# Kernel tuning notes

Measured on AMD Instinct MI355X. Metric: run time of the kernel, lower is better.

The kernel has to match this reference:

```python
import jax, jax.numpy as jnp
import numpy as np

N_NODES = 100000


def _prep(edge_index, n, dtype):
    # Add self-loops and compute GCN symmetric normalization (edge_weight = 1).
    loop = jnp.arange(n)
    src = jnp.concatenate([edge_index[0], loop])
    dst = jnp.concatenate([edge_index[1], loop])
    ones = jnp.ones(src.shape[0], dtype)
    deg = jax.ops.segment_sum(ones, dst, num_segments=n)  # in-degree over col, incl. self-loop
    dinv = jnp.where(deg > 0, 1.0 / jnp.sqrt(deg), 0.0)
    norm = dinv[src] * dinv[dst]  # per-edge deg^-1/2 * deg^-1/2
    cnt = jnp.maximum(deg, 1.0)   # incoming-edge count for aggr='mean' (weights are 1)
    return src, dst, norm, cnt


def _gcn_conv(h, W, b, src, dst, norm, cnt, n):
    # gather -> scale -> scatter-mean  (PyG GCNConv with aggr='mean')
    msg = norm[:, None] * (h @ W)[src]                      # [E+N, out]
    agg = jax.ops.segment_sum(msg, dst, num_segments=n)     # [N, out]
    return agg / cnt[:, None] + b


def setup_inputs() -> dict:
    key = jax.random.key(0)
    ks = jax.random.split(key, 8)
    n, d_in, d_h, d_out = N_NODES, 128, 128, 64
    x = jax.random.normal(ks[0], (n, d_in), dtype=jnp.float32)
    edge_index = jax.random.randint(ks[1], (2, 1600000), 0, n, dtype=jnp.int64)
    def glorot(k, fan_in, fan_out):
        s = jnp.sqrt(6.0 / (fan_in + fan_out)).astype(jnp.float32)
        return jax.random.uniform(k, (fan_in, fan_out), jnp.float32, -s, s)
    return {
        "x": x,
        "edge_index": edge_index,
        "W1": glorot(ks[2], d_in, d_h), "b1": jnp.zeros((d_h,), jnp.float32),
        "W2": glorot(ks[3], d_h, d_h), "b2": jnp.zeros((d_h,), jnp.float32),
        "W3": glorot(ks[4], d_h, d_out), "b3": jnp.zeros((d_out,), jnp.float32),
    }


def reference(x, edge_index, W1, b1, W2, b2, W3, b3):
    n = x.shape[0]
    src, dst, norm, cnt = _prep(edge_index, n, x.dtype)
    h = jax.nn.relu(_gcn_conv(x, W1, b1, src, dst, norm, cnt, n))  # dropout = identity (eval)
    h = jax.nn.relu(_gcn_conv(h, W2, b2, src, dst, norm, cnt, n))
    out = _gcn_conv(h, W3, b3, src, dst, norm, cnt, n)
    return out
```

## Files before the change

### kernel.cpp

```cpp
#include <hip/hip_runtime.h>
#include <hip/hip_fp16.h>
#include <math.h>


#define BLK 256

__global__ void init_and_pad(int* __restrict__ deg, int n,
                             int* __restrict__ colidx, int val, int len) {
    int i = blockIdx.x * blockDim.x + threadIdx.x;
    int stride = gridDim.x * blockDim.x;
    for (; i < len; i += stride) {
        if (i < n) deg[i] = 1;
        colidx[i] = val;
    }
}

__global__ void count_deg_rank(const int* __restrict__ dst, int* __restrict__ deg,
                               int* __restrict__ rank, int E) {
    int e = blockIdx.x * blockDim.x + threadIdx.x;
    if (e < E) {
        int old = atomicAdd(&deg[dst[e]], 1);
        rank[e] = old - 1;
    }
}

__device__ __forceinline__ int padcap(int d) { return (d - 1 + 7) & ~7; }

__global__ void scan_block_sums(const int* __restrict__ deg, int* __restrict__ bsum, int n) {
    __shared__ int s[BLK];
    int i = blockIdx.x * BLK + threadIdx.x;
    s[threadIdx.x] = (i < n) ? padcap(deg[i]) : 0;
    __syncthreads();
    for (int off = BLK / 2; off > 0; off >>= 1) {
        if (threadIdx.x < off) s[threadIdx.x] += s[threadIdx.x + off];
        __syncthreads();
    }
    if (threadIdx.x == 0) bsum[blockIdx.x] = s[0];
}

__global__ void scan_partials_excl(int* __restrict__ bsum, int nb) {
    __shared__ int a[512];
    __shared__ int b[512];
    int t = threadIdx.x;
    int v = (t < nb) ? bsum[t] : 0;
    a[t] = v;
    __syncthreads();
    int* s = a; int* d = b;
    for (int off = 1; off < 512; off <<= 1) {
        int val = s[t];
        if (t >= off) val += s[t - off];
        d[t] = val;
        __syncthreads();
        int* tmp = s; s = d; d = tmp;
    }
    if (t < nb) bsum[t] = s[t] - v;
}

__global__ void scan_write_rowptr(const int* __restrict__ deg, const int* __restrict__ bsum,
                                  int* __restrict__ rowptr, float* __restrict__ dinv, int n) {
    __shared__ int a[BLK];
    __shared__ int b[BLK];
    int t = threadIdx.x;
    int i = blockIdx.x * BLK + t;
    int dgv = (i < n) ? deg[i] : 1;
    int v = (i < n) ? padcap(dgv) : 0;
    a[t] = v;
    __syncthreads();
    int* s = a; int* d = b;
    for (int off = 1; off < BLK; off <<= 1) {
        int val = s[t];
        if (t >= off) val += s[t - off];
        d[t] = val;
        __syncthreads();
        int* tmp = s; s = d; d = tmp;
    }
    if (i < n) {
        rowptr[i] = (s[t] - v) + bsum[blockIdx.x];
        dinv[i] = 1.0f / sqrtf((float)dgv);
    }
}

__global__ void place_edges(const int* __restrict__ src, const int* __restrict__ dst,
                            const int* __restrict__ rowptr, const int* __restrict__ rank,
                            int* __restrict__ colidx, int E) {
    int e = blockIdx.x * blockDim.x + threadIdx.x;
    if (e < E) {
        int d = dst[e];
        colidx[rowptr[d] + rank[e]] = src[e];
    }
}

template <int KOUT>
__global__ __launch_bounds__(256) void gemm_tiled(const float* __restrict__ H,
                                                  const float* __restrict__ W,
                                                  const float* __restrict__ dinv,
                                                  __half* __restrict__ Y, int n) {
    constexpr int ROWS = (KOUT == 128) ? 64 : 128;
    constexpr int HSTR = 36;
    __shared__ float Hl[ROWS][HSTR];
    __shared__ float Wl[32][KOUT];

    const int t = threadIdx.x;
    const int wave = t >> 6, lane = t & 63;
    const int rg = lane >> 3;
    const int cg = lane & 7;
    const int rpanel = (KOUT == 128) ? (wave >> 1) : wave;
    const int cpanel = (KOUT == 128) ? (wave & 1) : 0;
    const int row0 = blockIdx.x * ROWS;
    const int cbase = cpanel * 64 + cg * 8;

    if (blockIdx.x == 0 && t < KOUT) Y[(size_t)n * KOUT + t] = __float2half(0.f);

    float acc[4][8];
#pragma unroll
    for (int i = 0; i < 4; i++)
#pragma unroll
        for (int j = 0; j < 8; j++) acc[i][j] = 0.f;

    for (int kt = 0; kt < 128; kt += 32) {
#pragma unroll
        for (int s = 0; s < ROWS / 32; s++) {
            int r = s * 32 + (t >> 3);
            int kk = (t & 7) * 4;
            int row = row0 + r;
            float4 v = make_float4(0.f, 0.f, 0.f, 0.f);
            if (row < n) v = *(const float4*)(H + (size_t)row * 128 + kt + kk);
            Hl[r][kk] = v.x; Hl[r][kk + 1] = v.y; Hl[r][kk + 2] = v.z; Hl[r][kk + 3] = v.w;
        }
        {
            const float* Wg = W + (size_t)kt * KOUT;
            float* Wf = &Wl[0][0];
            for (int idx = t * 4; idx < 32 * KOUT; idx += 1024) {
                *(float4*)(Wf + idx) = *(const float4*)(Wg + idx);
            }
        }
        __syncthreads();

#pragma unroll 2
        for (int kk = 0; kk < 32; kk += 4) {
            float4 a[4];
#pragma unroll
            for (int i = 0; i < 4; i++)
                a[i] = *(const float4*)(&Hl[rpanel * 32 + rg + 8 * i][kk]);
#pragma unroll
            for (int q = 0; q < 4; q++) {
                float4 w0 = *(const float4*)(&Wl[kk + q][cbase]);
                float4 w1 = *(const float4*)(&Wl[kk + q][cbase + 4]);
#pragma unroll
                for (int i = 0; i < 4; i++) {
                    float av = (q == 0) ? a[i].x : (q == 1) ? a[i].y : (q == 2) ? a[i].z : a[i].w;
                    acc[i][0] += av * w0.x; acc[i][1] += av * w0.y;
                    acc[i][2] += av * w0.z; acc[i][3] += av * w0.w;
                    acc[i][4] += av * w1.x; acc[i][5] += av * w1.y;
                    acc[i][6] += av * w1.z; acc[i][7] += av * w1.w;
                }
            }
        }
        __syncthreads();
    }

#pragma unroll
    for (int i = 0; i < 4; i++) {
        int row = row0 + rpanel * 32 + rg + 8 * i;
        if (row < n) {
            float dv = dinv[row];
            __half hv[8];
#pragma unroll
            for (int j = 0; j < 8; j++) hv[j] = __float2half_rn(dv * acc[i][j]);
            *(uint4*)(Y + (size_t)row * KOUT + cbase) = *(const uint4*)hv;
        }
    }
}

__device__ __forceinline__ int sel4(const int4 v, int q) {
    return (q == 0) ? v.x : (q == 1) ? v.y : (q == 2) ? v.z : v.w;
}

__device__ __forceinline__ void acc_half8(float* __restrict__ acc, const __half* __restrict__ p) {
    uint4 u = *(const uint4*)p;
    const __half2* h = (const __half2*)&u;
    float2 f0 = __half22float2(h[0]);
    float2 f1 = __half22float2(h[1]);
    float2 f2 = __half22float2(h[2]);
    float2 f3 = __half22float2(h[3]);
    acc[0] += f0.x; acc[1] += f0.y; acc[2] += f1.x; acc[3] += f1.y;
    acc[4] += f2.x; acc[5] += f2.y; acc[6] += f3.x; acc[7] += f3.y;
}

template <bool RELU>
__global__ __launch_bounds__(256) void agg128(const __half* __restrict__ Ys,
                                              const int* __restrict__ rowptr,
                                              const int* __restrict__ deg,
                                              const float* __restrict__ dinv,
                                              const int* __restrict__ colidx,
                                              const float* __restrict__ bias,
                                              float* __restrict__ out, int n) {
    int wid = (blockIdx.x * blockDim.x + threadIdx.x) >> 6;
    int lane = threadIdx.x & 63;
    if (wid >= n) return;
    const int q = lane >> 4;
    const int l4 = lane & 15;

    int start = __builtin_amdgcn_readfirstlane(rowptr[wid]);
    int dg    = __builtin_amdgcn_readfirstlane(deg[wid]);
    int mpad  = padcap(dg);
    float di = dinv[wid];

    float acc[8];
#pragma unroll
    for (int j = 0; j < 8; j++) acc[j] = 0.f;
    if (q == 0) acc_half8(acc, Ys + ((size_t)wid << 7) + l4 * 8);

    const int4* cp4 = (const int4*)(colidx + start);
    for (int j = 0; j < mpad; j += 8) {
        int4 a = cp4[j >> 2];
        int4 b = cp4[(j >> 2) + 1];
        int s0 = sel4(a, q);
        int s1 = sel4(b, q);
        acc_half8(acc, Ys + ((size_t)s0 << 7) + l4 * 8);
        acc_half8(acc, Ys + ((size_t)s1 << 7) + l4 * 8);
    }
#pragma unroll
    for (int j = 0; j < 8; j++) {
        acc[j] += __shfl_xor(acc[j], 16);
        acc[j] += __shfl_xor(acc[j], 32);
    }

    if (q == 0) {
        float scale = di / (float)dg;
        float4 b0 = *(const float4*)(bias + l4 * 8);
        float4 b1 = *(const float4*)(bias + l4 * 8 + 4);
        float o[8];
        o[0] = acc[0] * scale + b0.x; o[1] = acc[1] * scale + b0.y;
        o[2] = acc[2] * scale + b0.z; o[3] = acc[3] * scale + b0.w;
        o[4] = acc[4] * scale + b1.x; o[5] = acc[5] * scale + b1.y;
        o[6] = acc[6] * scale + b1.z; o[7] = acc[7] * scale + b1.w;
        if (RELU) {
#pragma unroll
            for (int j = 0; j < 8; j++) o[j] = fmaxf(o[j], 0.f);
        }
        float* op = out + ((size_t)wid << 7) + l4 * 8;
        *(float4*)op = make_float4(o[0], o[1], o[2], o[3]);
        *(float4*)(op + 4) = make_float4(o[4], o[5], o[6], o[7]);
    }
}

template <bool RELU>
__global__ __launch_bounds__(256) void agg64(const __half* __restrict__ Ys,
                                             const int* __restrict__ rowptr,
                                             const int* __restrict__ deg,
                                             const float* __restrict__ dinv,
                                             const int* __restrict__ colidx,
                                             const float* __restrict__ bias,
                                             float* __restrict__ out, int n) {
    int wid = (blockIdx.x * blockDim.x + threadIdx.x) >> 6;
    int lane = threadIdx.x & 63;
    if (wid >= n) return;
    const int oct = lane >> 3;
    const int l3 = lane & 7;

    int start = __builtin_amdgcn_readfirstlane(rowptr[wid]);
    int dg    = __builtin_amdgcn_readfirstlane(deg[wid]);
    int mpad  = padcap(dg);
    float di = dinv[wid];

    float acc[8];
#pragma unroll
    for (int j = 0; j < 8; j++) acc[j] = 0.f;
    if (oct == 0) acc_half8(acc, Ys + ((size_t)wid << 6) + l3 * 8);

    const int4* cp4 = (const int4*)(colidx + start);
    for (int j = 0; j < mpad; j += 8) {
        int4 a = cp4[j >> 2];
        int4 b = cp4[(j >> 2) + 1];
        int se = (oct < 4) ? sel4(a, oct) : sel4(b, oct - 4);
        acc_half8(acc, Ys + ((size_t)se << 6) + l3 * 8);
    }
#pragma unroll
    for (int j = 0; j < 8; j++) {
        acc[j] += __shfl_xor(acc[j], 8);
        acc[j] += __shfl_xor(acc[j], 16);
        acc[j] += __shfl_xor(acc[j], 32);
    }

    if (oct == 0) {
        float scale = di / (float)dg;
        float4 b0 = *(const float4*)(bias + l3 * 8);
        float4 b1 = *(const float4*)(bias + l3 * 8 + 4);
        float o[8];
        o[0] = acc[0] * scale + b0.x; o[1] = acc[1] * scale + b0.y;
        o[2] = acc[2] * scale + b0.z; o[3] = acc[3] * scale + b0.w;
        o[4] = acc[4] * scale + b1.x; o[5] = acc[5] * scale + b1.y;
        o[6] = acc[6] * scale + b1.z; o[7] = acc[7] * scale + b1.w;
        if (RELU) {
#pragma unroll
            for (int j = 0; j < 8; j++) o[j] = fmaxf(o[j], 0.f);
        }
        float* op = out + ((size_t)wid << 6) + l3 * 8;
        *(float4*)op = make_float4(o[0], o[1], o[2], o[3]);
        *(float4*)(op + 4) = make_float4(o[4], o[5], o[6], o[7]);
    }
}

extern "C" void kernel_launch(void* const* d_in, const int* in_sizes, int n_in,
                              void* d_out, int out_size, void* d_ws, size_t ws_size,
                              hipStream_t stream) {
    const float* x  = (const float*)d_in[0];
    const int*   ei = (const int*)d_in[1];
    const float* W1 = (const float*)d_in[2];
    const float* b1 = (const float*)d_in[3];
    const float* W2 = (const float*)d_in[4];
    const float* b2 = (const float*)d_in[5];
    const float* W3 = (const float*)d_in[6];
    const float* b3 = (const float*)d_in[7];
    float* out = (float*)d_out;

    const int n = in_sizes[0] / 128;
    const int E = in_sizes[1] / 2;
    const int* srcA = ei;
    const int* dstA = ei + E;
    const int Epad = E + 8 * n + 64;

    auto alignup = [](size_t v) { return (v + 255) & ~(size_t)255; };
    char* base = (char*)d_ws;
    size_t off = 0;
    int* deg    = (int*)(base + off); off = alignup(off + (size_t)n * 4);
    int* rank   = (int*)(base + off); off = alignup(off + (size_t)E * 4);
    int* rowptr = (int*)(base + off); off = alignup(off + (size_t)n * 4);
    int* bsum   = (int*)(base + off); off = alignup(off + (size_t)1024 * 4);
    int* colidx = (int*)(base + off); off = alignup(off + (size_t)Epad * 4);
    float* dinv = (float*)(base + off); off = alignup(off + (size_t)n * 4);
    float* Hb   = (float*)(base + off); off = alignup(off + (size_t)n * 128 * 4);
    __half* Yb  = (__half*)(base + off); off = alignup(off + (size_t)(n + 1) * 128 * 2);
    (void)ws_size;

    const int nbN = (n + BLK - 1) / BLK;
    const int nbE = (E + BLK - 1) / BLK;

    init_and_pad<<<2048, BLK, 0, stream>>>(deg, n, colidx, n, Epad);
    count_deg_rank<<<nbE, BLK, 0, stream>>>(dstA, deg, rank, E);
    scan_block_sums<<<nbN, BLK, 0, stream>>>(deg, bsum, n);
    scan_partials_excl<<<1, 512, 0, stream>>>(bsum, nbN);
    scan_write_rowptr<<<nbN, BLK, 0, stream>>>(deg, bsum, rowptr, dinv, n);
    place_edges<<<nbE, BLK, 0, stream>>>(srcA, dstA, rowptr, rank, colidx, E);

    const int aggBlocks = (n * 64 + BLK - 1) / BLK;

    gemm_tiled<128><<<(n + 63) / 64, 256, 0, stream>>>(x, W1, dinv, Yb, n);
    agg128<true><<<aggBlocks, BLK, 0, stream>>>(Yb, rowptr, deg, dinv, colidx, b1, Hb, n);

    gemm_tiled<128><<<(n + 63) / 64, 256, 0, stream>>>(Hb, W2, dinv, Yb, n);
    agg128<true><<<aggBlocks, BLK, 0, stream>>>(Yb, rowptr, deg, dinv, colidx, b2, Hb, n);

    gemm_tiled<64><<<(n + 127) / 128, 256, 0, stream>>>(Hb, W3, dinv, Yb, n);
    agg64<false><<<aggBlocks, BLK, 0, stream>>>(Yb, rowptr, deg, dinv, colidx, b3, out, n);
}
```

Measured before the change: 409.0 us.

## Use bf16 MFMA GEMMs, bf16 hidden activations, and batch atomic edge kernels

Replaces the FP32 tiled GEMMs with bf16 MFMA 16x16x32 kernels that read weights pre-transposed and cast by a new setup kernel. Hidden activations between layers are now stored as bf16 instead of fp32, which halves their memory traffic. The degree-count and edge-placement kernels now handle four edges per thread so more atomics and scattered loads are in flight at once. Rounding inputs and weights to bf16 lowers GEMM accuracy, and the MFMA epilogue writes scalar half values instead of vector stores.

```diff
diff --git a/kernel.cpp b/kernel.cpp
--- a/kernel.cpp
+++ b/kernel.cpp
@@ -4,6 +4,15 @@
 
 
 #define BLK 256
+
+typedef short bf16x8 __attribute__((ext_vector_type(8)));
+typedef float f32x4 __attribute__((ext_vector_type(4)));
+
+__device__ __forceinline__ unsigned short f2bf(float f) {
+    unsigned int u = __float_as_uint(f);
+    u += 0x7fffu + ((u >> 16) & 1u);
+    return (unsigned short)(u >> 16);
+}
 
 __global__ void init_and_pad(int* __restrict__ deg, int n,
                              int* __restrict__ colidx, int val, int len) {
@@ -15,13 +24,41 @@
     }
 }
 
+__global__ void transpose_cast_w3(const float* __restrict__ W1, const float* __restrict__ W2,
+                                  const float* __restrict__ W3, unsigned short* __restrict__ Wt1,
+                                  unsigned short* __restrict__ Wt2, unsigned short* __restrict__ Wt3) {
+    int idx = blockIdx.x * blockDim.x + threadIdx.x;
+    if (idx < 16384) {
+        int k = idx >> 7, c = idx & 127;
+        Wt1[c * 128 + k] = f2bf(W1[idx]);
+    } else if (idx < 32768) {
+        int j = idx - 16384; int k = j >> 7, c = j & 127;
+        Wt2[c * 128 + k] = f2bf(W2[j]);
+    } else if (idx < 40960) {
+        int j = idx - 32768; int k = j >> 6, c = j & 63;
+        Wt3[c * 128 + k] = f2bf(W3[j]);
+    }
+}
+
 __global__ void count_deg_rank(const int* __restrict__ dst, int* __restrict__ deg,
                                int* __restrict__ rank, int E) {
-    int e = blockIdx.x * blockDim.x + threadIdx.x;
-    if (e < E) {
-        int old = atomicAdd(&deg[dst[e]], 1);
-        rank[e] = old - 1;
-    }
+    int t = blockIdx.x * blockDim.x + threadIdx.x;
+    int s = gridDim.x * blockDim.x;
+    int e0 = t, e1 = t + s, e2 = t + 2 * s, e3 = t + 3 * s;
+    int d0 = 0, d1 = 0, d2 = 0, d3 = 0;
+    if (e0 < E) d0 = dst[e0];
+    if (e1 < E) d1 = dst[e1];
+    if (e2 < E) d2 = dst[e2];
+    if (e3 < E) d3 = dst[e3];
+    int r0 = 0, r1 = 0, r2 = 0, r3 = 0;
+    if (e0 < E) r0 = atomicAdd(&deg[d0], 1);
+    if (e1 < E) r1 = atomicAdd(&deg[d1], 1);
+    if (e2 < E) r2 = atomicAdd(&deg[d2], 1);
+    if (e3 < E) r3 = atomicAdd(&deg[d3], 1);
+    if (e0 < E) rank[e0] = r0 - 1;
+    if (e1 < E) rank[e1] = r1 - 1;
+    if (e2 < E) rank[e2] = r2 - 1;
+    if (e3 < E) rank[e3] = r3 - 1;
 }
 
 __device__ __forceinline__ int padcap(int d) { return (d - 1 + 7) & ~7; }
@@ -83,91 +120,95 @@
 __global__ void place_edges(const int* __restrict__ src, const int* __restrict__ dst,
                             const int* __restrict__ rowptr, const int* __restrict__ rank,
                             int* __restrict__ colidx, int E) {
-    int e = blockIdx.x * blockDim.x + threadIdx.x;
-    if (e < E) {
-        int d = dst[e];
-        colidx[rowptr[d] + rank[e]] = src[e];
-    }
-}
-
-template <int KOUT>
-__global__ __launch_bounds__(256) void gemm_tiled(const float* __restrict__ H,
-                                                  const float* __restrict__ W,
-                                                  const float* __restrict__ dinv,
-                                                  __half* __restrict__ Y, int n) {
-    constexpr int ROWS = (KOUT == 128) ? 64 : 128;
-    constexpr int HSTR = 36;
-    __shared__ float Hl[ROWS][HSTR];
-    __shared__ float Wl[32][KOUT];
-
+    int t = blockIdx.x * blockDim.x + threadIdx.x;
+    int s = gridDim.x * blockDim.x;
+    int e0 = t, e1 = t + s, e2 = t + 2 * s, e3 = t + 3 * s;
+    int d0 = 0, d1 = 0, d2 = 0, d3 = 0;
+    if (e0 < E) d0 = dst[e0];
+    if (e1 < E) d1 = dst[e1];
+    if (e2 < E) d2 = dst[e2];
+    if (e3 < E) d3 = dst[e3];
+    int p0 = 0, p1 = 0, p2 = 0, p3 = 0;
+    if (e0 < E) p0 = rowptr[d0] + rank[e0];
+    if (e1 < E) p1 = rowptr[d1] + rank[e1];
+    if (e2 < E) p2 = rowptr[d2] + rank[e2];
+    if (e3 < E) p3 = rowptr[d3] + rank[e3];
+    if (e0 < E) colidx[p0] = src[e0];
+    if (e1 < E) colidx[p1] = src[e1];
+    if (e2 < E) colidx[p2] = src[e2];
+    if (e3 < E) colidx[p3] = src[e3];
+}
+
+template <int KOUT, bool INF32>
+__global__ __launch_bounds__(256) void gemm_mfma(const void* __restrict__ Hv,
+                                                 const unsigned short* __restrict__ Wt,
+                                                 const float* __restrict__ dinv,
+                                                 __half* __restrict__ Y, int n) {
+    constexpr int NCH = KOUT / 16;
+    __shared__ unsigned short Hl[64][136];
+    __shared__ unsigned short Wl[KOUT][136];
     const int t = threadIdx.x;
+    const int row0 = blockIdx.x * 64;
+
+    for (int idx = t; idx < KOUT * 16; idx += 256) {
+        int r = idx >> 4, seg = idx & 15;
+        *(uint4*)&Wl[r][seg * 8] = *(const uint4*)(Wt + r * 128 + seg * 8);
+    }
+    if (INF32) {
+        const float* H = (const float*)Hv;
+        for (int idx = t; idx < 64 * 16; idx += 256) {
+            int r = idx >> 4, seg = idx & 15;
+            int row = row0 + r;
+            unsigned short tmp[8];
+            if (row < n) {
+                float4 v0 = *(const float4*)(H + (size_t)row * 128 + seg * 8);
+                float4 v1 = *(const float4*)(H + (size_t)row * 128 + seg * 8 + 4);
+                tmp[0] = f2bf(v0.x); tmp[1] = f2bf(v0.y); tmp[2] = f2bf(v0.z); tmp[3] = f2bf(v0.w);
+                tmp[4] = f2bf(v1.x); tmp[5] = f2bf(v1.y); tmp[6] = f2bf(v1.z); tmp[7] = f2bf(v1.w);
+            } else {
+#pragma unroll
+                for (int j = 0; j < 8; j++) tmp[j] = 0;
+            }
+            *(uint4*)&Hl[r][seg * 8] = *(const uint4*)tmp;
+        }
+    } else {
+        const unsigned short* H = (const unsigned short*)Hv;
+        for (int idx = t; idx < 64 * 16; idx += 256) {
+            int r = idx >> 4, seg = idx & 15;
+            int row = row0 + r;
+            uint4 v = make_uint4(0, 0, 0, 0);
+            if (row < n) v = *(const uint4*)(H + (size_t)row * 128 + seg * 8);
+            *(uint4*)&Hl[r][seg * 8] = v;
+        }
+    }
+    if (blockIdx.x == 0 && t < KOUT) Y[(size_t)n * KOUT + t] = __float2half(0.f);
+    __syncthreads();
+
     const int wave = t >> 6, lane = t & 63;
-    const int rg = lane >> 3;
-    const int cg = lane & 7;
-    const int rpanel = (KOUT == 128) ? (wave >> 1) : wave;
-    const int cpanel = (KOUT == 128) ? (wave & 1) : 0;
-    const int row0 = blockIdx.x * ROWS;
-    const int cbase = cpanel * 64 + cg * 8;
-
-    if (blockIdx.x == 0 && t < KOUT) Y[(size_t)n * KOUT + t] = __float2half(0.f);
-
-    float acc[4][8];
-#pragma unroll
-    for (int i = 0; i < 4; i++)
-#pragma unroll
-        for (int j = 0; j < 8; j++) acc[i][j] = 0.f;
-
-    for (int kt = 0; kt < 128; kt += 32) {
-#pragma unroll
-        for (int s = 0; s < ROWS / 32; s++) {
-            int r = s * 32 + (t >> 3);
-            int kk = (t & 7) * 4;
-            int row = row0 + r;
-            float4 v = make_float4(0.f, 0.f, 0.f, 0.f);
-            if (row < n) v = *(const float4*)(H + (size_t)row * 128 + kt + kk);
-            Hl[r][kk] = v.x; Hl[r][kk + 1] = v.y; Hl[r][kk + 2] = v.z; Hl[r][kk + 3] = v.w;
+    const int r16 = lane & 15, ko8 = (lane >> 4) * 8;
+    f32x4 acc[NCH];
+#pragma unroll
+    for (int c = 0; c < NCH; c++) acc[c] = (f32x4){0.f, 0.f, 0.f, 0.f};
+
+#pragma unroll
+    for (int kc = 0; kc < 4; kc++) {
+        bf16x8 a = *(const bf16x8*)&Hl[wave * 16 + r16][kc * 32 + ko8];
+#pragma unroll
+        for (int c = 0; c < NCH; c++) {
+            bf16x8 b = *(const bf16x8*)&Wl[c * 16 + r16][kc * 32 + ko8];
+            acc[c] = __builtin_amdgcn_mfma_f32_16x16x32_bf16(a, b, acc[c], 0, 0, 0);
         }
-        {
-            const float* Wg = W + (size_t)kt * KOUT;
-            float* Wf = &Wl[0][0];
-            for (int idx = t * 4; idx < 32 * KOUT; idx += 1024) {
-                *(float4*)(Wf + idx) = *(const float4*)(Wg + idx);
-            }
-        }
-        __syncthreads();
-
-#pragma unroll 2
-        for (int kk = 0; kk < 32; kk += 4) {
-            float4 a[4];
-#pragma unroll
-            for (int i = 0; i < 4; i++)
-                a[i] = *(const float4*)(&Hl[rpanel * 32 + rg + 8 * i][kk]);
-#pragma unroll
-            for (int q = 0; q < 4; q++) {
-                float4 w0 = *(const float4*)(&Wl[kk + q][cbase]);
-                float4 w1 = *(const float4*)(&Wl[kk + q][cbase + 4]);
-#pragma unroll
-                for (int i = 0; i < 4; i++) {
-                    float av = (q == 0) ? a[i].x : (q == 1) ? a[i].y : (q == 2) ? a[i].z : a[i].w;
-                    acc[i][0] += av * w0.x; acc[i][1] += av * w0.y;
-                    acc[i][2] += av * w0.z; acc[i][3] += av * w0.w;
-                    acc[i][4] += av * w1.x; acc[i][5] += av * w1.y;
-                    acc[i][6] += av * w1.z; acc[i][7] += av * w1.w;
-                }
-            }
-        }
-        __syncthreads();
-    }
-
-#pragma unroll
-    for (int i = 0; i < 4; i++) {
-        int row = row0 + rpanel * 32 + rg + 8 * i;
+    }
+
+    const int mbase = row0 + wave * 16 + (lane >> 4) * 4;
+#pragma unroll
+    for (int r = 0; r < 4; r++) {
+        int row = mbase + r;
         if (row < n) {
             float dv = dinv[row];
-            __half hv[8];
-#pragma unroll
-            for (int j = 0; j < 8; j++) hv[j] = __float2half_rn(dv * acc[i][j]);
-            *(uint4*)(Y + (size_t)row * KOUT + cbase) = *(const uint4*)hv;
+#pragma unroll
+            for (int c = 0; c < NCH; c++)
+                Y[(size_t)row * KOUT + c * 16 + r16] = __float2half_rn(acc[c][r] * dv);
         }
     }
 }
@@ -187,14 +228,13 @@
     acc[4] += f2.x; acc[5] += f2.y; acc[6] += f3.x; acc[7] += f3.y;
 }
 
-template <bool RELU>
 __global__ __launch_bounds__(256) void agg128(const __half* __restrict__ Ys,
                                               const int* __restrict__ rowptr,
                                               const int* __restrict__ deg,
                                               const float* __restrict__ dinv,
                                               const int* __restrict__ colidx,
                                               const float* __restrict__ bias,
-                                              float* __restrict__ out, int n) {
+                                              unsigned short* __restrict__ outb, int n) {
     int wid = (blockIdx.x * blockDim.x + threadIdx.x) >> 6;
     int lane = threadIdx.x & 63;
     if (wid >= n) return;
@@ -230,22 +270,19 @@
         float scale = di / (float)dg;
         float4 b0 = *(const float4*)(bias + l4 * 8);
         float4 b1 = *(const float4*)(bias + l4 * 8 + 4);
-        float o[8];
-        o[0] = acc[0] * scale + b0.x; o[1] = acc[1] * scale + b0.y;
-        o[2] = acc[2] * scale + b0.z; o[3] = acc[3] * scale + b0.w;
-        o[4] = acc[4] * scale + b1.x; o[5] = acc[5] * scale + b1.y;
-        o[6] = acc[6] * scale + b1.z; o[7] = acc[7] * scale + b1.w;
-        if (RELU) {
-#pragma unroll
-            for (int j = 0; j < 8; j++) o[j] = fmaxf(o[j], 0.f);
-        }
-        float* op = out + ((size_t)wid << 7) + l4 * 8;
-        *(float4*)op = make_float4(o[0], o[1], o[2], o[3]);
-        *(float4*)(op + 4) = make_float4(o[4], o[5], o[6], o[7]);
-    }
-}
-
-template <bool RELU>
+        unsigned short ob[8];
+        ob[0] = f2bf(fmaxf(acc[0] * scale + b0.x, 0.f));
+        ob[1] = f2bf(fmaxf(acc[1] * scale + b0.y, 0.f));
+        ob[2] = f2bf(fmaxf(acc[2] * scale + b0.z, 0.f));
+        ob[3] = f2bf(fmaxf(acc[3] * scale + b0.w, 0.f));
+        ob[4] = f2bf(fmaxf(acc[4] * scale + b1.x, 0.f));
+        ob[5] = f2bf(fmaxf(acc[5] * scale + b1.y, 0.f));
+        ob[6] = f2bf(fmaxf(acc[6] * scale + b1.z, 0.f));
+        ob[7] = f2bf(fmaxf(acc[7] * scale + b1.w, 0.f));
+        *(uint4*)(outb + ((size_t)wid << 7) + l4 * 8) = *(const uint4*)ob;
+    }
+}
+
 __global__ __launch_bounds__(256) void agg64(const __half* __restrict__ Ys,
                                              const int* __restrict__ rowptr,
                                              const int* __restrict__ deg,
@@ -292,10 +329,6 @@
         o[2] = acc[2] * scale + b0.z; o[3] = acc[3] * scale + b0.w;
         o[4] = acc[4] * scale + b1.x; o[5] = acc[5] * scale + b1.y;
         o[6] = acc[6] * scale + b1.z; o[7] = acc[7] * scale + b1.w;
-        if (RELU) {
-#pragma unroll
-            for (int j = 0; j < 8; j++) o[j] = fmaxf(o[j], 0.f);
-        }
         float* op = out + ((size_t)wid << 6) + l3 * 8;
         *(float4*)op = make_float4(o[0], o[1], o[2], o[3]);
         *(float4*)(op + 4) = make_float4(o[4], o[5], o[6], o[7]);
@@ -330,28 +363,33 @@
     int* bsum   = (int*)(base + off); off = alignup(off + (size_t)1024 * 4);
     int* colidx = (int*)(base + off); off = alignup(off + (size_t)Epad * 4);
     float* dinv = (float*)(base + off); off = alignup(off + (size_t)n * 4);
-    float* Hb   = (float*)(base + off); off = alignup(off + (size_t)n * 128 * 4);
+    unsigned short* Wt1 = (unsigned short*)(base + off); off = alignup(off + 16384 * 2);
+    unsigned short* Wt2 = (unsigned short*)(base + off); off = alignup(off + 16384 * 2);
+    unsigned short* Wt3 = (unsigned short*)(base + off); off = alignup(off + 8192 * 2);
+    unsigned short* Hb  = (unsigned short*)(base + off); off = alignup(off + (size_t)n * 128 * 2);
     __half* Yb  = (__half*)(base + off); off = alignup(off + (size_t)(n + 1) * 128 * 2);
     (void)ws_size;
 
     const int nbN = (n + BLK - 1) / BLK;
-    const int nbE = (E + BLK - 1) / BLK;
+    const int nbE4 = (E + BLK * 4 - 1) / (BLK * 4);
 
     init_and_pad<<<2048, BLK, 0, stream>>>(deg, n, colidx, n, Epad);
-    count_deg_rank<<<nbE, BLK, 0, stream>>>(dstA, deg, rank, E);
+    transpose_cast_w3<<<160, BLK, 0, stream>>>(W1, W2, W3, Wt1, Wt2, Wt3);
+    count_deg_rank<<<nbE4, BLK, 0, stream>>>(dstA, deg, rank, E);
     scan_block_sums<<<nbN, BLK, 0, stream>>>(deg, bsum, n);
     scan_partials_excl<<<1, 512, 0, stream>>>(bsum, nbN);
     scan_write_rowptr<<<nbN, BLK, 0, stream>>>(deg, bsum, rowptr, dinv, n);
-    place_edges<<<nbE, BLK, 0, stream>>>(srcA, dstA, rowptr, rank, colidx, E);
+    place_edges<<<nbE4, BLK, 0, stream>>>(srcA, dstA, rowptr, rank, colidx, E);
 
     const int aggBlocks = (n * 64 + BLK - 1) / BLK;
-
-    gemm_tiled<128><<<(n + 63) / 64, 256, 0, stream>>>(x, W1, dinv, Yb, n);
-    agg128<true><<<aggBlocks, BLK, 0, stream>>>(Yb, rowptr, deg, dinv, colidx, b1, Hb, n);
-
-    gemm_tiled<128><<<(n + 63) / 64, 256, 0, stream>>>(Hb, W2, dinv, Yb, n);
-    agg128<true><<<aggBlocks, BLK, 0, stream>>>(Yb, rowptr, deg, dinv, colidx, b2, Hb, n);
-
-    gemm_tiled<64><<<(n + 127) / 128, 256, 0, stream>>>(Hb, W3, dinv, Yb, n);
-    agg64<false><<<aggBlocks, BLK, 0, stream>>>(Yb, rowptr, deg, dinv, colidx, b3, out, n);
-}
+    const int gemmBlocks = (n + 63) / 64;
+
+    gemm_mfma<128, true><<<gemmBlocks, 256, 0, stream>>>(x, Wt1, dinv, Yb, n);
+    agg128<<<aggBlocks, BLK, 0, stream>>>(Yb, rowptr, deg, dinv, colidx, b1, Hb, n);
+
+    gemm_mfma<128, false><<<gemmBlocks, 256, 0, stream>>>(Hb, Wt2, dinv, Yb, n);
+    agg128<<<aggBlocks, BLK, 0, stream>>>(Yb, rowptr, deg, dinv, colidx, b2, Hb, n);
+
+    gemm_mfma<64, false><<<gemmBlocks, 256, 0, stream>>>(Hb, Wt3, dinv, Yb, n);
+    agg64<<<aggBlocks, BLK, 0, stream>>>(Yb, rowptr, deg, dinv, colidx, b3, out, n);
+}
```

Result: faster. 345.4 us (-15.6%).
